# Performance work log

Hardware: AMD Instinct MI355X
Metric: run time of the kernel (lower is better)

Reference implementation:

```python
import jax, jax.numpy as jnp
import numpy as np

B, T, S, D = 8, 16, 256, 1024
H, KVH, HD = 16, 4, 64
GROUPS = H // KVH
SCALE = HD ** -0.5
CAP = 50.0
EPS = 1e-6


def setup_inputs() -> dict:
    key = jax.random.key(0)
    ks = jax.random.split(key, 5)
    return {
        "x": jax.random.normal(ks[0], (B, T, S, D), dtype=jnp.float32),
        "Wq": jax.random.normal(ks[1], (D, H * HD), dtype=jnp.float32) * (D ** -0.5),
        "Wk": jax.random.normal(ks[2], (D, KVH * HD), dtype=jnp.float32) * (D ** -0.5),
        "Wv": jax.random.normal(ks[3], (D, KVH * HD), dtype=jnp.float32) * (D ** -0.5),
        "Wo": jax.random.normal(ks[4], (H * HD, D), dtype=jnp.float32) * ((H * HD) ** -0.5),
        "q_norm_w": jnp.ones((HD,), dtype=jnp.float32),
        "k_norm_w": jnp.ones((HD,), dtype=jnp.float32),
    }


def _rmsnorm(x, w):
    rms = jnp.sqrt(jnp.mean(x * x, axis=-1, keepdims=True) + EPS)
    return x / rms * w


def reference(x, Wq, Wk, Wv, Wo, q_norm_w, k_norm_w):
    b, t, s, d = x.shape
    xf = x.reshape(b * t, s, d)                    # (BT, S, D)
    q = (xf @ Wq).reshape(b * t, s, H, HD).transpose(0, 2, 1, 3)   # (BT, H, S, hd)
    k = (xf @ Wk).reshape(b * t, s, KVH, HD).transpose(0, 2, 1, 3)  # (BT, KVH, S, hd)
    v = (xf @ Wv).reshape(b * t, s, KVH, HD).transpose(0, 2, 1, 3)
    q = _rmsnorm(q, q_norm_w)
    k = _rmsnorm(k, k_norm_w)
    if GROUPS > 1:
        k = jnp.repeat(k, GROUPS, axis=1)          # (BT, H, S, hd)
        v = jnp.repeat(v, GROUPS, axis=1)
    logits = jnp.einsum("bhqd,bhkd->bhqk", q, k) * SCALE
    logits = CAP * jnp.tanh(logits / CAP)          # soft cap
    attn = jax.nn.softmax(logits, axis=-1)
    out = jnp.einsum("bhqk,bhkd->bhqd", attn, v)   # (BT, H, S, hd)
    out = out.transpose(0, 2, 1, 3).reshape(b * t, s, H * HD)
    out = out @ Wo
    return out.reshape(b, t, s, d)
```

## Files before the change

### kernel.cpp

```cpp
#include <hip/hip_runtime.h>
#include <cstdint>
#include <cstddef>

typedef __bf16 bf16x8 __attribute__((ext_vector_type(8)));
typedef float f32x4 __attribute__((ext_vector_type(4)));
typedef unsigned short u16;
typedef unsigned int u32;
typedef unsigned short u16x8 __attribute__((ext_vector_type(8)));

#define ROWS 32768
#define DMODEL 1024
#define NQKV 1536
#define C1_ 0.0072134752044448170f
#define A2_ 144.26950408889634f
#define B2_ 72.13475204444817f

__device__ __forceinline__ u16 f2bf(float f) {
    unsigned u = __float_as_uint(f);
    u += 0x7fffu + ((u >> 16) & 1u);
    return (u16)(u >> 16);
}
__device__ __forceinline__ float bf_lo(u32 u) { return __uint_as_float(u << 16); }
__device__ __forceinline__ float bf_hi(u32 u) { return __uint_as_float(u & 0xffff0000u); }
__device__ __forceinline__ u32 pack_rne(float lo, float hi) {
    return (u32)f2bf(lo) | ((u32)f2bf(hi) << 16);
}

__global__ __launch_bounds__(256) void f32_to_bf16_vec(
    const float* __restrict__ in, u16* __restrict__ out, int n4)
{
    int i = blockIdx.x * 256 + threadIdx.x;
    if (i >= n4) return;
    float4 f = ((const float4*)in)[i];
    ushort4 u;
    u.x = f2bf(f.x); u.y = f2bf(f.y); u.z = f2bf(f.z); u.w = f2bf(f.w);
    ((ushort4*)out)[i] = u;
}

__global__ __launch_bounds__(256) void transpose_bf16(
    const float* __restrict__ src, u16* __restrict__ dst, int R, int C)
{
    __shared__ float tile[32][33];
    int c0 = blockIdx.x * 32;
    int r0 = blockIdx.y * 32;
    int tx = threadIdx.x & 31;
    int ty = threadIdx.x >> 5;
#pragma unroll
    for (int i = 0; i < 32; i += 8)
        tile[ty + i][tx] = src[(size_t)(r0 + ty + i) * C + (c0 + tx)];
    __syncthreads();
#pragma unroll
    for (int i = 0; i < 32; i += 8)
        dst[(size_t)(c0 + ty + i) * R + (r0 + tx)] = f2bf(tile[tx][ty + i]);
}

template<bool BF16OUT>
__global__ __launch_bounds__(256) void gemm_bt(
    const u16* __restrict__ A, const u16* __restrict__ Bt,
    void* __restrict__ Cout, int M, int N, int K)
{
    __shared__ u16 As[128][32];
    __shared__ u16 Bs[128][32];
    const int tid  = threadIdx.x;
    const int wave = tid >> 6;
    const int lane = tid & 63;
    const int q4   = lane >> 4;
    const int cl   = lane & 15;
    const int wr   = wave >> 1, wc = wave & 1;
    const int m0   = blockIdx.x * 128;
    const int n0   = blockIdx.y * 128;
    const int srow = lane >> 2;
    const int skoff = (lane & 3) * 8;

    const f32x4 zero = {0.f, 0.f, 0.f, 0.f};
    f32x4 acc[4][4];
#pragma unroll
    for (int i = 0; i < 4; ++i)
#pragma unroll
        for (int j = 0; j < 4; ++j) acc[i][j] = zero;

    for (int k0 = 0; k0 < K; k0 += 32) {
        __syncthreads();
#pragma unroll
        for (int cc = 0; cc < 2; ++cc) {
            int r = 32 * wave + 16 * cc + srow;
            const u16* ga = A + (size_t)(m0 + r) * K + k0 + skoff;
            __builtin_amdgcn_global_load_lds(
                (const __attribute__((address_space(1))) void*)ga,
                (__attribute__((address_space(3))) void*)(&As[32 * wave + 16 * cc][0]),
                16, 0, 0);
            const u16* gb = Bt + (size_t)(n0 + r) * K + k0 + skoff;
            __builtin_amdgcn_global_load_lds(
                (const __attribute__((address_space(1))) void*)gb,
                (__attribute__((address_space(3))) void*)(&Bs[32 * wave + 16 * cc][0]),
                16, 0, 0);
        }
        __syncthreads();
        bf16x8 af[4], bfr[4];
#pragma unroll
        for (int i = 0; i < 4; ++i)
            af[i] = *(const bf16x8*)&As[64 * wr + 16 * i + cl][q4 * 8];
#pragma unroll
        for (int j = 0; j < 4; ++j)
            bfr[j] = *(const bf16x8*)&Bs[64 * wc + 16 * j + cl][q4 * 8];
#pragma unroll
        for (int i = 0; i < 4; ++i)
#pragma unroll
            for (int j = 0; j < 4; ++j)
                acc[i][j] = __builtin_amdgcn_mfma_f32_16x16x32_bf16(
                    af[i], bfr[j], acc[i][j], 0, 0, 0);
    }

#pragma unroll
    for (int i = 0; i < 4; ++i)
#pragma unroll
        for (int j = 0; j < 4; ++j)
#pragma unroll
            for (int r = 0; r < 4; ++r) {
                int row = m0 + 64 * wr + 16 * i + q4 * 4 + r;
                int col = n0 + 64 * wc + 16 * j + cl;
                if (BF16OUT)
                    ((u16*)Cout)[(size_t)row * N + col] = f2bf(acc[i][j][r]);
                else
                    ((float*)Cout)[(size_t)row * N + col] = acc[i][j][r];
            }
}

__global__ __launch_bounds__(256, 3) void attention_kernel(
    const u16* __restrict__ qkv, const float* __restrict__ qw,
    const float* __restrict__ kw, u16* __restrict__ ao)
{
    const int bi  = blockIdx.x;
    const int bt  = bi >> 4;
    const int h   = bi & 15;
    const int kvh = h >> 2;
    const int tid  = threadIdx.x;
    const int wave = tid >> 6;
    const int lane = tid & 63;
    const int q4   = lane >> 4;
    const int cl   = lane & 15;

    __shared__ __align__(16) u16 Vt[64][264];
    __shared__ __align__(16) u16 P[4][64][40];

    {
        const u16* vrow = qkv + (size_t)(bt * 256 + tid) * NQKV + 1280 + kvh * 64;
#pragma unroll
        for (int ch = 0; ch < 8; ++ch) {
            u16x8 v8 = *(const u16x8*)(vrow + ch * 8);
#pragma unroll
            for (int e = 0; e < 8; ++e) Vt[ch * 8 + e][tid] = v8[e];
        }
    }
    __syncthreads();

    const u16* qbase = qkv + (size_t)(bt * 256) * NQKV + h * 64;
    const u16* kbase = qkv + (size_t)(bt * 256) * NQKV + 1024 + kvh * 64;

    uint4 qa[2][4];
    float rq[4];
    float wqk[2][8];
#pragma unroll
    for (int ks = 0; ks < 2; ++ks)
#pragma unroll
        for (int e = 0; e < 8; ++e) {
            int d = ks * 32 + q4 * 8 + e;
            wqk[ks][e] = qw[d] * kw[d];
        }
#pragma unroll
    for (int i = 0; i < 4; ++i) {
#pragma unroll
        for (int ks = 0; ks < 2; ++ks)
            qa[ks][i] = *(const uint4*)(qbase +
                (size_t)(wave * 64 + 16 * i + cl) * NQKV + ks * 32 + q4 * 8);
        float ss = 0.f;
#pragma unroll
        for (int ks = 0; ks < 2; ++ks) {
            const u32* u = (const u32*)&qa[ks][i];
#pragma unroll
            for (int e = 0; e < 4; ++e) {
                float lo = bf_lo(u[e]), hi = bf_hi(u[e]);
                ss += lo * lo + hi * hi;
            }
        }
        ss += __shfl_xor(ss, 16, 64);
        ss += __shfl_xor(ss, 32, 64);
        rq[i] = rsqrtf(ss * (1.0f / 64.0f) + 1e-6f);
#pragma unroll
        for (int ks = 0; ks < 2; ++ks) {
            u32* u = (u32*)&qa[ks][i];
#pragma unroll
            for (int e = 0; e < 4; ++e) {
                float lo = bf_lo(u[e]) * wqk[ks][2 * e];
                float hi = bf_hi(u[e]) * wqk[ks][2 * e + 1];
                u[e] = pack_rne(lo, hi);
            }
        }
    }
    float rqc[4][4];
#pragma unroll
    for (int i = 0; i < 4; ++i)
#pragma unroll
        for (int r = 0; r < 4; ++r)
            rqc[i][r] = __shfl(rq[i], 4 * q4 + r, 64);

    const f32x4 zero = {0.f, 0.f, 0.f, 0.f};
    f32x4 o[4][4];
    f32x4 lacc[4];
#pragma unroll
    for (int i = 0; i < 4; ++i) {
        lacc[i] = zero;
#pragma unroll
        for (int j = 0; j < 4; ++j) o[i][j] = zero;
    }
    bf16x8 ones;
#pragma unroll
    for (int e = 0; e < 8; ++e) ones[e] = (__bf16)1.0f;

    for (int nb = 0; nb < 4; ++nb) {
#pragma unroll
        for (int jh = 0; jh < 2; ++jh) {
#pragma unroll
            for (int jj = 0; jj < 2; ++jj) {
                const int j = 2 * jh + jj;
                uint4 kb[2];
#pragma unroll
                for (int ks = 0; ks < 2; ++ks)
                    kb[ks] = *(const uint4*)(kbase +
                        (size_t)(nb * 64 + 16 * j + cl) * NQKV + ks * 32 + q4 * 8);
                float ss = 0.f;
#pragma unroll
                for (int ks = 0; ks < 2; ++ks) {
                    const u32* u = (const u32*)&kb[ks];
#pragma unroll
                    for (int e = 0; e < 4; ++e) {
                        float lo = bf_lo(u[e]), hi = bf_hi(u[e]);
                        ss += lo * lo + hi * hi;
                    }
                }
                ss += __shfl_xor(ss, 16, 64);
                ss += __shfl_xor(ss, 32, 64);
                float rkc1 = rsqrtf(ss * (1.0f / 64.0f) + 1e-6f) * C1_;

#pragma unroll
                for (int i = 0; i < 4; ++i) {
                    f32x4 s = __builtin_amdgcn_mfma_f32_16x16x32_bf16(
                        *(const bf16x8*)&qa[0][i], *(const bf16x8*)&kb[0], zero, 0, 0, 0);
                    s = __builtin_amdgcn_mfma_f32_16x16x32_bf16(
                        *(const bf16x8*)&qa[1][i], *(const bf16x8*)&kb[1], s, 0, 0, 0);
#pragma unroll
                    for (int r = 0; r < 4; ++r) {
                        float e2 = __builtin_amdgcn_exp2f(s[r] * rqc[i][r] * rkc1);
                        float rc = __builtin_amdgcn_rcpf(e2 + 1.0f);
                        float p  = __builtin_amdgcn_exp2f(fmaf(-A2_, rc, B2_));
                        P[wave][16 * i + q4 * 4 + r][16 * jj + cl] = f2bf(p);
                    }
                }
            }
            bf16x8 vb[4];
#pragma unroll
            for (int j2 = 0; j2 < 4; ++j2)
                vb[j2] = *(const bf16x8*)&Vt[16 * j2 + cl][nb * 64 + jh * 32 + q4 * 8];
#pragma unroll
            for (int i = 0; i < 4; ++i) {
                bf16x8 pa = *(const bf16x8*)&P[wave][16 * i + cl][q4 * 8];
#pragma unroll
                for (int j2 = 0; j2 < 4; ++j2)
                    o[i][j2] = __builtin_amdgcn_mfma_f32_16x16x32_bf16(
                        pa, vb[j2], o[i][j2], 0, 0, 0);
                lacc[i] = __builtin_amdgcn_mfma_f32_16x16x32_bf16(
                    pa, ones, lacc[i], 0, 0, 0);
            }
        }
    }

#pragma unroll
    for (int i = 0; i < 4; ++i)
#pragma unroll
        for (int r = 0; r < 4; ++r) {
            float inv = 1.0f / lacc[i][r];
            int row = bt * 256 + wave * 64 + 16 * i + q4 * 4 + r;
#pragma unroll
            for (int j = 0; j < 4; ++j) {
                int col = h * 64 + 16 * j + cl;
                ao[(size_t)row * DMODEL + col] = f2bf(o[i][j][r] * inv);
            }
        }
}

extern "C" void kernel_launch(void* const* d_in, const int* in_sizes, int n_in,
                              void* d_out, int out_size, void* d_ws, size_t ws_size,
                              hipStream_t stream)
{
    const float* x  = (const float*)d_in[0];
    const float* Wq = (const float*)d_in[1];
    const float* Wk = (const float*)d_in[2];
    const float* Wv = (const float*)d_in[3];
    const float* Wo = (const float*)d_in[4];
    const float* qw = (const float*)d_in[5];
    const float* kw = (const float*)d_in[6];
    float* out = (float*)d_out;

    char* ws = (char*)d_ws;
    u16* Xb  = (u16*)(ws);
    u16* QKV = (u16*)(ws + (size_t)67108864);
    u16* AO  = (u16*)(ws + (size_t)167772160);
    u16* WcT = (u16*)(ws + (size_t)234881024);
    u16* WoT = (u16*)(ws + (size_t)238026752);

    f32_to_bf16_vec<<<dim3(32768), dim3(256), 0, stream>>>(x, Xb, 8388608);
    transpose_bf16<<<dim3(32, 32), dim3(256), 0, stream>>>(Wq, WcT, 1024, 1024);
    transpose_bf16<<<dim3(8, 32), dim3(256), 0, stream>>>(Wk, WcT + (size_t)1024 * 1024, 1024, 256);
    transpose_bf16<<<dim3(8, 32), dim3(256), 0, stream>>>(Wv, WcT + (size_t)1280 * 1024, 1024, 256);
    transpose_bf16<<<dim3(32, 32), dim3(256), 0, stream>>>(Wo, WoT, 1024, 1024);
    gemm_bt<true><<<dim3(256, 12), dim3(256), 0, stream>>>(Xb, WcT, (void*)QKV, ROWS, NQKV, 1024);
    attention_kernel<<<dim3(2048), dim3(256), 0, stream>>>(QKV, qw, kw, AO);
    gemm_bt<false><<<dim3(256, 8), dim3(256), 0, stream>>>(AO, WoT, (void*)out, ROWS, DMODEL, 1024);
}
```

Baseline: 659.6 us.

## Swizzle block order per XCD, prefetch K tiles, and stage attention output

The GEMM blocks are remapped so that consecutive logical tiles, which share A rows, land on the same XCD (blocks are dealt round-robin across 8 dies). The attention block index gets the same remap so all heads of one bt share an XCD's L2 for K/V. In attention, Q loads are issued before the V transpose, and K tiles are software-prefetched one step ahead to hide global latency. The output is staged through LDS with an XOR swizzle so it can be written as 16-byte coalesced stores instead of scattered 2-byte stores. This costs extra registers, which could lower occupancy, and adds one more barrier.

```diff
diff --git a/kernel.cpp b/kernel.cpp
--- a/kernel.cpp
+++ b/kernel.cpp
@@ -54,7 +54,7 @@
         dst[(size_t)(c0 + ty + i) * R + (r0 + tx)] = f2bf(tile[tx][ty + i]);
 }
 
-template<bool BF16OUT>
+template<bool BF16OUT, int NY>
 __global__ __launch_bounds__(256) void gemm_bt(
     const u16* __restrict__ A, const u16* __restrict__ Bt,
     void* __restrict__ Cout, int M, int N, int K)
@@ -67,8 +67,11 @@
     const int q4   = lane >> 4;
     const int cl   = lane & 15;
     const int wr   = wave >> 1, wc = wave & 1;
-    const int m0   = blockIdx.x * 128;
-    const int n0   = blockIdx.y * 128;
+    const int id   = blockIdx.y * gridDim.x + blockIdx.x;
+    const int cpx  = (gridDim.x * gridDim.y) >> 3;
+    const int swz  = (id & 7) * cpx + (id >> 3);
+    const int m0   = (swz / NY) * 128;
+    const int n0   = (swz % NY) * 128;
     const int srow = lane >> 2;
     const int skoff = (lane & 3) * 8;
 
@@ -130,9 +133,9 @@
     const u16* __restrict__ qkv, const float* __restrict__ qw,
     const float* __restrict__ kw, u16* __restrict__ ao)
 {
-    const int bi  = blockIdx.x;
-    const int bt  = bi >> 4;
-    const int h   = bi & 15;
+    const int lg  = (blockIdx.x & 7) * 256 + (blockIdx.x >> 3);
+    const int bt  = lg >> 4;
+    const int h   = lg & 15;
     const int kvh = h >> 2;
     const int tid  = threadIdx.x;
     const int wave = tid >> 6;
@@ -143,6 +146,17 @@
     __shared__ __align__(16) u16 Vt[64][264];
     __shared__ __align__(16) u16 P[4][64][40];
 
+    const u16* qbase = qkv + (size_t)(bt * 256) * NQKV + h * 64;
+    const u16* kbase = qkv + (size_t)(bt * 256) * NQKV + 1024 + kvh * 64;
+
+    uint4 qa[2][4];
+#pragma unroll
+    for (int i = 0; i < 4; ++i)
+#pragma unroll
+        for (int ks = 0; ks < 2; ++ks)
+            qa[ks][i] = *(const uint4*)(qbase +
+                (size_t)(wave * 64 + 16 * i + cl) * NQKV + ks * 32 + q4 * 8);
+
     {
         const u16* vrow = qkv + (size_t)(bt * 256 + tid) * NQKV + 1280 + kvh * 64;
 #pragma unroll
@@ -154,10 +168,10 @@
     }
     __syncthreads();
 
-    const u16* qbase = qkv + (size_t)(bt * 256) * NQKV + h * 64;
-    const u16* kbase = qkv + (size_t)(bt * 256) * NQKV + 1024 + kvh * 64;
-
-    uint4 qa[2][4];
+    uint4 kcur0 = *(const uint4*)(kbase + (size_t)cl * NQKV + q4 * 8);
+    uint4 kcur1 = *(const uint4*)(kbase + (size_t)cl * NQKV + 32 + q4 * 8);
+    uint4 knxt0, knxt1;
+
     float rq[4];
     float wqk[2][8];
 #pragma unroll
@@ -169,10 +183,6 @@
         }
 #pragma unroll
     for (int i = 0; i < 4; ++i) {
-#pragma unroll
-        for (int ks = 0; ks < 2; ++ks)
-            qa[ks][i] = *(const uint4*)(qbase +
-                (size_t)(wave * 64 + 16 * i + cl) * NQKV + ks * 32 + q4 * 8);
         float ss = 0.f;
 #pragma unroll
         for (int ks = 0; ks < 2; ++ks) {
@@ -222,19 +232,21 @@
         for (int jh = 0; jh < 2; ++jh) {
 #pragma unroll
             for (int jj = 0; jj < 2; ++jj) {
-                const int j = 2 * jh + jj;
-                uint4 kb[2];
-#pragma unroll
-                for (int ks = 0; ks < 2; ++ks)
-                    kb[ks] = *(const uint4*)(kbase +
-                        (size_t)(nb * 64 + 16 * j + cl) * NQKV + ks * 32 + q4 * 8);
+                const int t = nb * 4 + 2 * jh + jj;
+                if (t < 15) {
+                    int rown = ((t + 1) >> 2) * 64 + 16 * ((t + 1) & 3) + cl;
+                    knxt0 = *(const uint4*)(kbase + (size_t)rown * NQKV + q4 * 8);
+                    knxt1 = *(const uint4*)(kbase + (size_t)rown * NQKV + 32 + q4 * 8);
+                }
                 float ss = 0.f;
-#pragma unroll
-                for (int ks = 0; ks < 2; ++ks) {
-                    const u32* u = (const u32*)&kb[ks];
+                {
+                    const u32* u0 = (const u32*)&kcur0;
+                    const u32* u1 = (const u32*)&kcur1;
 #pragma unroll
                     for (int e = 0; e < 4; ++e) {
-                        float lo = bf_lo(u[e]), hi = bf_hi(u[e]);
+                        float lo = bf_lo(u0[e]), hi = bf_hi(u0[e]);
+                        ss += lo * lo + hi * hi;
+                        lo = bf_lo(u1[e]); hi = bf_hi(u1[e]);
                         ss += lo * lo + hi * hi;
                     }
                 }
@@ -245,9 +257,9 @@
 #pragma unroll
                 for (int i = 0; i < 4; ++i) {
                     f32x4 s = __builtin_amdgcn_mfma_f32_16x16x32_bf16(
-                        *(const bf16x8*)&qa[0][i], *(const bf16x8*)&kb[0], zero, 0, 0, 0);
+                        *(const bf16x8*)&qa[0][i], *(const bf16x8*)&kcur0, zero, 0, 0, 0);
                     s = __builtin_amdgcn_mfma_f32_16x16x32_bf16(
-                        *(const bf16x8*)&qa[1][i], *(const bf16x8*)&kb[1], s, 0, 0, 0);
+                        *(const bf16x8*)&qa[1][i], *(const bf16x8*)&kcur1, s, 0, 0, 0);
 #pragma unroll
                     for (int r = 0; r < 4; ++r) {
                         float e2 = __builtin_amdgcn_exp2f(s[r] * rqc[i][r] * rkc1);
@@ -256,6 +268,7 @@
                         P[wave][16 * i + q4 * 4 + r][16 * jj + cl] = f2bf(p);
                     }
                 }
+                if (t < 15) { kcur0 = knxt0; kcur1 = knxt1; }
             }
             bf16x8 vb[4];
 #pragma unroll
@@ -274,18 +287,27 @@
         }
     }
 
+    __syncthreads();
+    u16* st = (u16*)Vt + wave * 4096;
 #pragma unroll
     for (int i = 0; i < 4; ++i)
 #pragma unroll
         for (int r = 0; r < 4; ++r) {
             float inv = 1.0f / lacc[i][r];
-            int row = bt * 256 + wave * 64 + 16 * i + q4 * 4 + r;
-#pragma unroll
-            for (int j = 0; j < 4; ++j) {
-                int col = h * 64 + 16 * j + cl;
-                ao[(size_t)row * DMODEL + col] = f2bf(o[i][j][r] * inv);
-            }
-        }
+            int row = 16 * i + 4 * q4 + r;
+            int sw  = q4 << 4;
+#pragma unroll
+            for (int j = 0; j < 4; ++j)
+                st[row * 64 + ((16 * j + cl) ^ sw)] = f2bf(o[i][j][r] * inv);
+        }
+#pragma unroll
+    for (int it = 0; it < 8; ++it) {
+        int lr = it * 8 + (lane >> 3);
+        int cb = lane & 7;
+        int sw = ((lr >> 2) & 3) << 4;
+        uint4 val = *(const uint4*)&st[lr * 64 + ((cb * 8) ^ sw)];
+        *(uint4*)(ao + (size_t)(bt * 256 + wave * 64 + lr) * DMODEL + h * 64 + cb * 8) = val;
+    }
 }
 
 extern "C" void kernel_launch(void* const* d_in, const int* in_sizes, int n_in,
@@ -313,7 +335,7 @@
     transpose_bf16<<<dim3(8, 32), dim3(256), 0, stream>>>(Wk, WcT + (size_t)1024 * 1024, 1024, 256);
     transpose_bf16<<<dim3(8, 32), dim3(256), 0, stream>>>(Wv, WcT + (size_t)1280 * 1024, 1024, 256);
     transpose_bf16<<<dim3(32, 32), dim3(256), 0, stream>>>(Wo, WoT, 1024, 1024);
-    gemm_bt<true><<<dim3(256, 12), dim3(256), 0, stream>>>(Xb, WcT, (void*)QKV, ROWS, NQKV, 1024);
+    gemm_bt<true, 12><<<dim3(256, 12), dim3(256), 0, stream>>>(Xb, WcT, (void*)QKV, ROWS, NQKV, 1024);
     attention_kernel<<<dim3(2048), dim3(256), 0, stream>>>(QKV, qw, kw, AO);
-    gemm_bt<false><<<dim3(256, 8), dim3(256), 0, stream>>>(AO, WoT, (void*)out, ROWS, DMODEL, 1024);
-}
+    gemm_bt<false, 8><<<dim3(256, 8), dim3(256), 0, stream>>>(AO, WoT, (void*)out, ROWS, DMODEL, 1024);
+}
```

New measurement: 688.6 us. +4.4%, slower.
